# Performance work log

Measured on AMD Instinct MI355X. Metric: run time of the kernel, lower is better.

Reference implementation:

```python
import jax, jax.numpy as jnp
import numpy as np

MARGIN = 1.0
EPS = 1e-11


def setup_inputs() -> dict:
    key = jax.random.key(0)
    k1, k2, k3 = jax.random.split(key, 3)
    B, D, C = 8192, 512, 128
    features = jax.random.normal(k1, (B, D), dtype=jnp.float32)
    labels = jax.random.randint(k2, (B,), 0, C, dtype=jnp.int64)
    neg_u = jax.random.uniform(k3, (B,), dtype=jnp.float32)
    return {"features": features, "labels": labels, "neg_u": neg_u}


def reference(features, labels, neg_u):
    n = features.shape[0]
    sq = jnp.sum(features * features, axis=1)  # [n]
    d2 = sq[:, None] + sq[None, :] - 2.0 * (features @ features.T)
    dist = jnp.sqrt(jnp.clip(d2, EPS, None))  # [n, n]

    same = labels[:, None] == labels[None, :]
    eye = jnp.eye(n, dtype=bool)
    pos_mask = same & ~eye           # valid positives per anchor
    neg_mask = ~same                 # valid negatives per anchor
    n_neg = neg_mask.sum(axis=1)     # [n]

    # deterministic "random" negative: pick the floor(u * n_neg)-th negative
    # (stable argsort puts negatives first, preserving original order)
    order = jnp.argsort(jnp.where(neg_mask, 0, 1), axis=1, stable=True)  # [n, n]
    k = jnp.floor(neg_u * n_neg.astype(neg_u.dtype)).astype(jnp.int32)
    k = jnp.clip(k, 0, jnp.maximum(n_neg - 1, 0).astype(jnp.int32))
    neg_idx = jnp.take_along_axis(order, k[:, None], axis=1)[:, 0]       # [n]
    neg_dist = dist[jnp.arange(n), neg_idx]                               # [n]

    # MarginRankingLoss(y=1): max(0, margin + pos_dist - neg_dist), per (anchor, pos) pair
    valid = pos_mask & (n_neg > 0)[:, None]
    per_pair = jnp.maximum(MARGIN + dist - neg_dist[:, None], 0.0)
    counter = valid.sum()
    total = jnp.where(valid, per_pair, 0.0).sum()
    return total / counter.astype(total.dtype)
```

## Files before the change

### kernel.cpp

```cpp
#include <hip/hip_runtime.h>
#include <hip/hip_bf16.h>
#include <cstdint>

#define NN 8192
#define DD 512
#define NC 128

typedef unsigned short u16;
typedef __attribute__((ext_vector_type(8))) short short8;
typedef __attribute__((ext_vector_type(4))) float f32x4;

#define AS1 __attribute__((address_space(1)))
#define AS3 __attribute__((address_space(3)))

__device__ __forceinline__ float bf2f(short x) {
  return __uint_as_float(((unsigned)(unsigned short)x) << 16);
}

#define FB_OFF   ((size_t)0)
#define SQ_OFF   (FB_OFF + (size_t)NN*DD*2)
#define ACC_OFF  (SQ_OFF + (size_t)NN*4)
#define CC_OFF   (ACC_OFF + 64)
#define POS_OFF  (CC_OFF + 1024)

__global__ __launch_bounds__(256) void k_pc(const float* __restrict__ F,
    const int* __restrict__ labels, u16* __restrict__ Fb,
    float* __restrict__ sq, int* __restrict__ cc, int* __restrict__ pos,
    int* __restrict__ accz) {
  const int wid = threadIdx.x >> 6, lane = threadIdx.x & 63;
  if (blockIdx.x < 2048) {
    if (blockIdx.x == 0 && threadIdx.x < 16) accz[threadIdx.x] = 0;
    const int row = blockIdx.x * 4 + wid;
    const float* fr = F + (size_t)row * DD + lane * 8;
    float4 v0 = *(const float4*)fr;
    float4 v1 = *(const float4*)(fr + 4);
    float s = v0.x*v0.x + v0.y*v0.y + v0.z*v0.z + v0.w*v0.w
            + v1.x*v1.x + v1.y*v1.y + v1.z*v1.z + v1.w*v1.w;
    #pragma unroll
    for (int o = 32; o; o >>= 1) s += __shfl_xor(s, o);
    float t[8] = {v0.x, v0.y, v0.z, v0.w, v1.x, v1.y, v1.z, v1.w};
    unsigned p[8];
    #pragma unroll
    for (int e = 0; e < 8; ++e) {
      unsigned b = __float_as_uint(t[e]);
      b += 0x7fffu + ((b >> 16) & 1u);
      p[e] = b >> 16;
    }
    uint4 w;
    w.x = p[0] | (p[1] << 16); w.y = p[2] | (p[3] << 16);
    w.z = p[4] | (p[5] << 16); w.w = p[6] | (p[7] << 16);
    *(uint4*)(Fb + (size_t)row * DD + lane * 8) = w;
    if (lane == 0) sq[row] = s;
  } else {
    const int c = blockIdx.x - 2048;
    __shared__ int wcnt[4], woff[4];
    const int base0 = wid * 2048;
    int cw = 0;
    for (int b = 0; b < 2048; b += 64)
      cw += __popcll(__ballot(labels[base0 + b + lane] == c));
    if (lane == 0) wcnt[wid] = cw;
    __syncthreads();
    if (threadIdx.x == 0) {
      int o = 0;
      #pragma unroll
      for (int w = 0; w < 4; ++w) { woff[w] = o; o += wcnt[w]; }
      cc[c] = o;
    }
    __syncthreads();
    int off = woff[wid];
    for (int b = 0; b < 2048; b += 64) {
      const int idx = base0 + b + lane;
      const int hit = (labels[idx] == c);
      const unsigned long long m = __ballot(hit);
      if (hit) pos[c * 128 + off + __popcll(m & ((1ull << lane) - 1ull))] = idx;
      off += __popcll(m);
    }
    __syncthreads();
    const int nc = cc[c];
    for (int t = nc + threadIdx.x; t < 128; t += 256) pos[c * 128 + t] = 0;
  }
}

__global__ __launch_bounds__(256) void k_cls(const u16* __restrict__ Fb,
    const float* __restrict__ sq, const float* __restrict__ negu,
    const int* __restrict__ cc, const int* __restrict__ pos,
    float* __restrict__ accf, float* __restrict__ out) {
  const int c = blockIdx.x & 127, half = blockIdx.x >> 7;
  __shared__ __align__(16) u16 P[128 * 512];
  __shared__ int posc[128], jm[64];
  __shared__ float pd[64][4], ndc[64], sqc[128];
  __shared__ float red[4];
  const int tid = threadIdx.x, wid = tid >> 6, lane = tid & 63;
  const int nc = cc[c];
  if (tid < 128) posc[tid] = pos[c * 128 + tid];
  __syncthreads();
  if (nc >= 2 && half * 64 < nc) {
    const int wr = half, wc = wid;
    const int r16 = lane & 15, gg = lane >> 4;
    const char* fb = (const char*)Fb;

    #pragma unroll 8
    for (int s = 0; s < 32; ++s) {
      const int row = wid * 32 + s;
      const int gr = posc[row];
      __builtin_amdgcn_global_load_lds(
          (const AS1 void*)(fb + (size_t)gr * 1024 + ((lane ^ (s & 7)) << 4)),
          (AS3 void*)(&P[row * 512]), 16, 0, 0);
    }

    if (tid < 128) sqc[tid] = sq[posc[tid]];

    {
      const int ml = tid >> 2, q = tid & 3;
      const int row = half * 64 + ml;
      if (row < nc) {
        const int i = posc[row];
        const int n_neg = NN - nc;
        int k = (int)floorf(negu[i] * (float)n_neg);
        k = k < 0 ? 0 : (k > n_neg - 1 ? n_neg - 1 : k);
        int lo = 0, hi = nc;
        while (lo < hi) {
          const int mid = (lo + hi) >> 1;
          if (posc[mid] - mid <= k) lo = mid + 1; else hi = mid;
        }
        const int j = k + lo;
        if (q == 0) jm[ml] = j;
        const u16* fi = Fb + (size_t)i * DD + q * 128;
        const u16* fj = Fb + (size_t)j * DD + q * 128;
        float d = 0.0f;
        #pragma unroll 4
        for (int e = 0; e < 16; ++e) {
          const short8 a = ((const short8*)fi)[e];
          const short8 b = ((const short8*)fj)[e];
          #pragma unroll
          for (int x = 0; x < 8; ++x) d += bf2f(a[x]) * bf2f(b[x]);
        }
        pd[ml][q] = d;
      }
    }

    f32x4 acc[4][2];
    #pragma unroll
    for (int m = 0; m < 4; ++m)
      #pragma unroll
      for (int n = 0; n < 2; ++n)
        #pragma unroll
        for (int q = 0; q < 4; ++q) acc[m][n][q] = 0.0f;

    __syncthreads();
    if (tid < 64) {
      const int row = half * 64 + tid;
      if (row < nc) {
        const float d = pd[tid][0] + pd[tid][1] + pd[tid][2] + pd[tid][3];
        ndc[tid] = sqrtf(fmaxf(sqc[row] + sq[jm[tid]] - 2.0f * d, 1e-11f));
      } else ndc[tid] = __builtin_inff();
    }

    #pragma unroll 4
    for (int t = 0; t < 16; ++t) {
      short8 af[4], bf[2];
      #pragma unroll
      for (int m = 0; m < 4; ++m) {
        const int row = wr * 64 + m * 16 + r16;
        const int gl = (t * 4 + gg) ^ (row & 7);
        af[m] = *(const short8*)&P[row * 512 + gl * 8];
      }
      #pragma unroll
      for (int n = 0; n < 2; ++n) {
        const int row = wc * 32 + n * 16 + r16;
        const int gl = (t * 4 + gg) ^ (row & 7);
        bf[n] = *(const short8*)&P[row * 512 + gl * 8];
      }
      #pragma unroll
      for (int m = 0; m < 4; ++m)
        #pragma unroll
        for (int n = 0; n < 2; ++n)
          acc[m][n] = __builtin_amdgcn_mfma_f32_16x16x32_bf16(af[m], bf[n], acc[m][n], 0, 0, 0);
    }
    __syncthreads();

    float lsum = 0.0f;
    int njv[2]; float sqj[2];
    #pragma unroll
    for (int n = 0; n < 2; ++n) {
      const int nj = wc * 32 + n * 16 + r16;
      njv[n] = nj; sqj[n] = sqc[nj];
    }
    #pragma unroll
    for (int m = 0; m < 4; ++m) {
      #pragma unroll
      for (int q = 0; q < 4; ++q) {
        const int mi = wr * 64 + m * 16 + gg * 4 + q;
        const float sqi = sqc[mi];
        const float ndi = ndc[mi - half * 64];
        const bool vi = mi < nc;
        #pragma unroll
        for (int n = 0; n < 2; ++n) {
          const float g = acc[m][n][q];
          const float dist = sqrtf(fmaxf(sqi + sqj[n] - 2.0f * g, 1e-11f));
          if (vi & (njv[n] < nc) & (mi != njv[n]))
            lsum += fmaxf(1.0f + dist - ndi, 0.0f);
        }
      }
    }
    #pragma unroll
    for (int o = 32; o; o >>= 1) lsum += __shfl_xor(lsum, o);
    if (lane == 0) red[wid] = lsum;
    __syncthreads();
    if (tid == 0) atomicAdd(accf, red[0] + red[1] + red[2] + red[3]);
  }
  if (tid == 0) {
    int* cnt  = (int*)accf + 1;
    int* done = (int*)accf + 2;
    if (half == 0 && nc < NN) atomicAdd(cnt, nc * (nc - 1));
    __threadfence();
    if (atomicAdd(done, 1) == 2 * NC - 1) {
      const float tot = atomicAdd(accf, 0.0f);
      const int n = atomicAdd(cnt, 0);
      out[0] = tot / (float)n;
    }
  }
}

extern "C" void kernel_launch(void* const* d_in, const int* in_sizes, int n_in,
                              void* d_out, int out_size, void* d_ws, size_t ws_size,
                              hipStream_t stream) {
  const float* F = (const float*)d_in[0];
  const int* labels = (const int*)d_in[1];
  const float* negu = (const float*)d_in[2];
  char* ws = (char*)d_ws;
  u16*   Fb    = (u16*)(ws + FB_OFF);
  float* sq    = (float*)(ws + SQ_OFF);
  float* accf  = (float*)(ws + ACC_OFF);
  int*   cc    = (int*)(ws + CC_OFF);
  int*   pos   = (int*)(ws + POS_OFF);

  k_pc <<<2048 + NC, 256, 0, stream>>>(F, labels, Fb, sq, cc, pos, (int*)accf);
  k_cls<<<2 * NC,    256, 0, stream>>>(Fb, sq, negu, cc, pos, accf, (float*)d_out);
}
```

Measured before the change: 33.50 us.

## Process each class in one 512-thread block instead of two half blocks

Merges the two per-class blocks into a single 512-thread block whose eight waves cover the full 128x128 gram tile. Each class's feature rows are loaded into LDS once instead of twice, and the negative-distance setup covers all 128 rows. The trade-off is half as many blocks in the grid, leaving more CUs idle.

After: 34.11 us. About the same (+1.8%).

```diff
diff --git a/kernel.cpp b/kernel.cpp
--- a/kernel.cpp
+++ b/kernel.cpp
@@ -81,30 +81,30 @@
   }
 }
 
-__global__ __launch_bounds__(256) void k_cls(const u16* __restrict__ Fb,
+__global__ __launch_bounds__(512) void k_cls(const u16* __restrict__ Fb,
     const float* __restrict__ sq, const float* __restrict__ negu,
     const int* __restrict__ cc, const int* __restrict__ pos,
     float* __restrict__ accf, float* __restrict__ out) {
-  const int c = blockIdx.x & 127, half = blockIdx.x >> 7;
+  const int c = blockIdx.x;
   __shared__ __align__(16) u16 P[128 * 512];
-  __shared__ int posc[128], jm[64];
-  __shared__ float pd[64][4], ndc[64], sqc[128];
-  __shared__ float red[4];
+  __shared__ int posc[128], jm[128];
+  __shared__ float pd[128][4], ndc[128], sqc[128];
+  __shared__ float red[8];
   const int tid = threadIdx.x, wid = tid >> 6, lane = tid & 63;
   const int nc = cc[c];
   if (tid < 128) posc[tid] = pos[c * 128 + tid];
   __syncthreads();
-  if (nc >= 2 && half * 64 < nc) {
-    const int wr = half, wc = wid;
+  if (nc >= 2) {
+    const int wr = wid >> 2, wc = wid & 3;
     const int r16 = lane & 15, gg = lane >> 4;
     const char* fb = (const char*)Fb;
 
-    #pragma unroll 8
-    for (int s = 0; s < 32; ++s) {
-      const int row = wid * 32 + s;
+    #pragma unroll 4
+    for (int s = 0; s < 16; ++s) {
+      const int row = wid * 16 + s;
       const int gr = posc[row];
       __builtin_amdgcn_global_load_lds(
-          (const AS1 void*)(fb + (size_t)gr * 1024 + ((lane ^ (s & 7)) << 4)),
+          (const AS1 void*)(fb + (size_t)gr * 1024 + ((lane ^ (row & 7)) << 4)),
           (AS3 void*)(&P[row * 512]), 16, 0, 0);
     }
 
@@ -112,9 +112,8 @@
 
     {
       const int ml = tid >> 2, q = tid & 3;
-      const int row = half * 64 + ml;
-      if (row < nc) {
-        const int i = posc[row];
+      if (ml < nc) {
+        const int i = posc[ml];
         const int n_neg = NN - nc;
         int k = (int)floorf(negu[i] * (float)n_neg);
         k = k < 0 ? 0 : (k > n_neg - 1 ? n_neg - 1 : k);
@@ -148,11 +147,10 @@
         for (int q = 0; q < 4; ++q) acc[m][n][q] = 0.0f;
 
     __syncthreads();
-    if (tid < 64) {
-      const int row = half * 64 + tid;
-      if (row < nc) {
+    if (tid < 128) {
+      if (tid < nc) {
         const float d = pd[tid][0] + pd[tid][1] + pd[tid][2] + pd[tid][3];
-        ndc[tid] = sqrtf(fmaxf(sqc[row] + sq[jm[tid]] - 2.0f * d, 1e-11f));
+        ndc[tid] = sqrtf(fmaxf(sqc[tid] + sq[jm[tid]] - 2.0f * d, 1e-11f));
       } else ndc[tid] = __builtin_inff();
     }
 
@@ -192,7 +190,7 @@
       for (int q = 0; q < 4; ++q) {
         const int mi = wr * 64 + m * 16 + gg * 4 + q;
         const float sqi = sqc[mi];
-        const float ndi = ndc[mi - half * 64];
+        const float ndi = ndc[mi];
         const bool vi = mi < nc;
         #pragma unroll
         for (int n = 0; n < 2; ++n) {
@@ -207,14 +205,19 @@
     for (int o = 32; o; o >>= 1) lsum += __shfl_xor(lsum, o);
     if (lane == 0) red[wid] = lsum;
     __syncthreads();
-    if (tid == 0) atomicAdd(accf, red[0] + red[1] + red[2] + red[3]);
+    if (tid == 0) {
+      float s = 0.0f;
+      #pragma unroll
+      for (int w = 0; w < 8; ++w) s += red[w];
+      atomicAdd(accf, s);
+    }
   }
   if (tid == 0) {
     int* cnt  = (int*)accf + 1;
     int* done = (int*)accf + 2;
-    if (half == 0 && nc < NN) atomicAdd(cnt, nc * (nc - 1));
+    if (nc < NN) atomicAdd(cnt, nc * (nc - 1));
     __threadfence();
-    if (atomicAdd(done, 1) == 2 * NC - 1) {
+    if (atomicAdd(done, 1) == NC - 1) {
       const float tot = atomicAdd(accf, 0.0f);
       const int n = atomicAdd(cnt, 0);
       out[0] = tot / (float)n;
@@ -236,5 +239,5 @@
   int*   pos   = (int*)(ws + POS_OFF);
 
   k_pc <<<2048 + NC, 256, 0, stream>>>(F, labels, Fb, sq, cc, pos, (int*)accf);
-  k_cls<<<2 * NC,    256, 0, stream>>>(Fb, sq, negu, cc, pos, accf, (float*)d_out);
-}
+  k_cls<<<NC,        512, 0, stream>>>(Fb, sq, negu, cc, pos, accf, (float*)d_out);
+}
```
